# Kernel optimization log

Hardware: AMD Instinct MI355X
Metric: run time of the kernel (lower is better)

## Reference

```python
import jax, jax.numpy as jnp
import numpy as np

HEADS = 4
KS = 7          # neighborhood kernel size
EPS = 1e-5
C = 64
N, H, W = 8, 64, 64


def _gather_idx(L, k):
    # NATTEN-style neighborhood: window centered at pixel, shifted to stay in bounds.
    start = jnp.clip(jnp.arange(L) - k // 2, 0, L - k)            # [L]
    idx = start[:, None] + jnp.arange(k)                           # [L, k] absolute neighbor idx
    # relative-position-bias index: (query - neighbor) + (k-1) in [0, 2k-2]
    rel = (jnp.arange(L) - start)[:, None] + (k - 1) - jnp.arange(k)[None, :]  # [L, k]
    return idx, rel


def na2d(x, qkv_w, qkv_b, rpb, proj_w, proj_b):
    # x: [N, H, W, C] -> neighborhood attention with rel-pos bias
    n, h, w, c = x.shape
    hd = c // HEADS
    scale = hd ** -0.5
    qkv = (x @ qkv_w.T + qkv_b).reshape(n, h, w, 3, HEADS, hd)
    q = qkv[..., 0, :, :] * scale                                  # [n,h,w,heads,hd]
    k = qkv[..., 1, :, :]
    v = qkv[..., 2, :, :]
    idx_h, rel_h = _gather_idx(h, KS)
    idx_w, rel_w = _gather_idx(w, KS)
    # gather neighborhoods: [n, h, k, w, k, heads, hd]
    kg = k[:, idx_h][:, :, :, idx_w]
    vg = v[:, idx_h][:, :, :, idx_w]
    attn = jnp.einsum('nijhd,niajbhd->nijhab', q, kg)              # [n,h,w,heads,k,k]
    bias = rpb[:, rel_h, :]                                        # [heads, h, k, 2k-1]
    bias = jnp.take(bias, rel_w, axis=-1)                          # [heads, h, k, w, k]
    bias = jnp.transpose(bias, (1, 3, 0, 2, 4))                    # [h, w, heads, k, k]
    attn = attn + bias
    a = jax.nn.softmax(attn.reshape(n, h, w, HEADS, KS * KS), axis=-1).reshape(attn.shape)
    out = jnp.einsum('nijhab,niajbhd->nijhd', a, vg).reshape(n, h, w, c)
    return out @ proj_w.T + proj_b


def setup_inputs() -> dict:
    key = jax.random.key(0)
    ks = jax.random.split(key, 12)
    s = 0.02
    return {
        'x': jax.random.normal(ks[0], (N, C, H, W), jnp.float32),
        'gn_w': jnp.ones((C,), jnp.float32),
        'gn_b': jnp.zeros((C,), jnp.float32),
        'qkv_w': jax.random.normal(ks[1], (3 * C, C), jnp.float32) * s,
        'qkv_b': jnp.zeros((3 * C,), jnp.float32),
        'rpb': jax.random.normal(ks[2], (HEADS, 2 * KS - 1, 2 * KS - 1), jnp.float32) * s,
        'proj_w': jax.random.normal(ks[3], (C, C), jnp.float32) * s,
        'proj_b': jnp.zeros((C,), jnp.float32),
        'ln_w': jnp.ones((C,), jnp.float32),
        'ln_b': jnp.zeros((C,), jnp.float32),
        'fc1_w': jax.random.normal(ks[4], (4 * C, C), jnp.float32) * s,
        'fc1_b': jnp.zeros((4 * C,), jnp.float32),
        'fc2_w': jax.random.normal(ks[5], (C, 4 * C), jnp.float32) * s,
        'fc2_b': jnp.zeros((C,), jnp.float32),
    }


def reference(x, gn_w, gn_b, qkv_w, qkv_b, rpb, proj_w, proj_b,
              ln_w, ln_b, fc1_w, fc1_b, fc2_w, fc2_b):
    n, c, h, w = x.shape
    x1 = jnp.transpose(x, (0, 2, 3, 1))                            # residual, NHWC
    # GroupNorm(1, C): normalize over (C,H,W) per sample, per-channel affine
    mu = jnp.mean(x, axis=(1, 2, 3), keepdims=True)
    var = jnp.var(x, axis=(1, 2, 3), keepdims=True)
    xg = (x - mu) * jax.lax.rsqrt(var + EPS)
    xg = xg * gn_w[None, :, None, None] + gn_b[None, :, None, None]
    xg = jnp.transpose(xg, (0, 2, 3, 1))                           # NHWC
    y = na2d(xg, qkv_w, qkv_b, rpb, proj_w, proj_b) + x1           # [n,h,w,c]
    y = y.reshape(n, h * w, c)
    # LayerNorm over channels + MLP (GELU), residual
    mu2 = jnp.mean(y, axis=-1, keepdims=True)
    var2 = jnp.var(y, axis=-1, keepdims=True)
    yn = (y - mu2) * jax.lax.rsqrt(var2 + EPS) * ln_w + ln_b
    hdn = jax.nn.gelu(yn @ fc1_w.T + fc1_b, approximate=False)
    y = y + (hdn @ fc2_w.T + fc2_b)
    return jnp.transpose(y.reshape(n, h, w, c), (0, 3, 1, 2))      # back to NCHW
```

## Files before the change

kernel.cpp:

```cpp
#include <hip/hip_runtime.h>
#include <math.h>

#define NSAMP 8
#define CH 64
#define HH 64
#define WW 64
#define SPATIAL 4096
#define PER_SAMPLE 262144
#define NTOK 32768
#define NHEADS 4
#define HD 16
#define KS 7
#define EPS 1e-5f
#define QSCALE 0.25f

typedef __attribute__((ext_vector_type(8))) short short8;
typedef __attribute__((ext_vector_type(4))) float f32x4;

__device__ __forceinline__ unsigned short f2bf(float f) {
    unsigned u = __float_as_uint(f);
    u = u + 0x7fffu + ((u >> 16) & 1u);
    return (unsigned short)(u >> 16);
}
__device__ __forceinline__ unsigned pack2(float a, float b) {
    return (unsigned)f2bf(a) | ((unsigned)f2bf(b) << 16);
}
__device__ __forceinline__ float dot8_bf(uint4 u, const float* qv) {
    float s;
    s = __uint_as_float(u.x << 16) * qv[0];
    s = fmaf(__uint_as_float(u.x & 0xffff0000u), qv[1], s);
    s = fmaf(__uint_as_float(u.y << 16),         qv[2], s);
    s = fmaf(__uint_as_float(u.y & 0xffff0000u), qv[3], s);
    s = fmaf(__uint_as_float(u.z << 16),         qv[4], s);
    s = fmaf(__uint_as_float(u.z & 0xffff0000u), qv[5], s);
    s = fmaf(__uint_as_float(u.w << 16),         qv[6], s);
    s = fmaf(__uint_as_float(u.w & 0xffff0000u), qv[7], s);
    return s;
}
__device__ __forceinline__ void pv8_bf(uint4 u, float p, float* acc) {
    acc[0] = fmaf(p, __uint_as_float(u.x << 16),         acc[0]);
    acc[1] = fmaf(p, __uint_as_float(u.x & 0xffff0000u), acc[1]);
    acc[2] = fmaf(p, __uint_as_float(u.y << 16),         acc[2]);
    acc[3] = fmaf(p, __uint_as_float(u.y & 0xffff0000u), acc[3]);
    acc[4] = fmaf(p, __uint_as_float(u.z << 16),         acc[4]);
    acc[5] = fmaf(p, __uint_as_float(u.z & 0xffff0000u), acc[5]);
    acc[6] = fmaf(p, __uint_as_float(u.w << 16),         acc[6]);
    acc[7] = fmaf(p, __uint_as_float(u.w & 0xffff0000u), acc[7]);
}

__global__ __launch_bounds__(256) void k_statsprep(const float* __restrict__ x,
                                                   float* __restrict__ stats,
                                                   const float* __restrict__ qkv_w,
                                                   const float* __restrict__ fc1_w,
                                                   const float* __restrict__ fc2_w,
                                                   const float* __restrict__ proj_w,
                                                   unsigned short* __restrict__ wb) {
    int blk = blockIdx.x;
    if (blk >= 256) {
        int i = (blk - 256) * 256 + threadIdx.x;
        if (i < 12288)      wb[i] = f2bf(qkv_w[i]);
        else if (i < 28672) wb[i] = f2bf(fc1_w[i - 12288]);
        else if (i < 45056) wb[i] = f2bf(fc2_w[i - 28672]);
        else                wb[i] = f2bf(proj_w[i - 45056]);
        return;
    }
    int n = blk >> 5, chunk = blk & 31;
    const float4* p4 = (const float4*)(x + n * PER_SAMPLE + chunk * 8192);
    int t = threadIdx.x;
    float s1 = 0.f, s2 = 0.f;
#pragma unroll
    for (int i = 0; i < 8; i++) {
        float4 v = p4[t + i * 256];
        s1 += v.x + v.y + v.z + v.w;
        s2 += v.x * v.x + v.y * v.y + v.z * v.z + v.w * v.w;
    }
#pragma unroll
    for (int off = 1; off < 64; off <<= 1) {
        s1 += __shfl_xor(s1, off);
        s2 += __shfl_xor(s2, off);
    }
    __shared__ float r1[4], r2[4];
    int lane = t & 63, wv = t >> 6;
    if (lane == 0) { r1[wv] = s1; r2[wv] = s2; }
    __syncthreads();
    if (t == 0) {
        atomicAdd(&stats[n * 2 + 0], r1[0] + r1[1] + r1[2] + r1[3]);
        atomicAdd(&stats[n * 2 + 1], r2[0] + r2[1] + r2[2] + r2[3]);
    }
}

__global__ __launch_bounds__(256) void k_qkv(const float* __restrict__ x,
                                             const float* __restrict__ stats,
                                             const float* __restrict__ gn_w,
                                             const float* __restrict__ gn_b,
                                             const unsigned short* __restrict__ qkv_wb,
                                             const float* __restrict__ qkv_b,
                                             uint4* __restrict__ qb8,
                                             uint4* __restrict__ kvb8) {
    __shared__ __attribute__((aligned(16))) short xA[4 * 2 * 64 * 8];
    __shared__ float obuf[4][16 * 65];
    int s0 = blockIdx.x * 64;
    int smp = s0 >> 12, sp = s0 & 4095;
    int t = threadIdx.x, tok = t & 63, g = t >> 6;

    float mu = stats[2 * smp] * (1.f / (float)PER_SAMPLE);
    float var = stats[2 * smp + 1] * (1.f / (float)PER_SAMPLE) - mu * mu;
    float rstd = rsqrtf(var + EPS);

    {
        const float* xp = x + smp * PER_SAMPLE + sp + tok;
        float v[16];
#pragma unroll
        for (int i = 0; i < 16; i++) {
            int c = g * 16 + i;
            v[i] = (xp[(size_t)c * SPATIAL] - mu) * rstd * gn_w[c] + gn_b[c];
        }
#pragma unroll
        for (int e = 0; e < 2; e++) {
            int cb = 2 * g + e;
            int kf = cb >> 2, qq = cb & 3;
            uint4 p;
            p.x = pack2(v[e * 8 + 0], v[e * 8 + 1]);
            p.y = pack2(v[e * 8 + 2], v[e * 8 + 3]);
            p.z = pack2(v[e * 8 + 4], v[e * 8 + 5]);
            p.w = pack2(v[e * 8 + 6], v[e * 8 + 7]);
            int chunk = ((tok >> 4) * 2 + kf) * 64 + (tok & 15) + (qq << 4);
            *(uint4*)&xA[chunk * 8] = p;
        }
    }
    __syncthreads();

    int w = __builtin_amdgcn_readfirstlane(g);
    int lane = t & 63, nh = lane & 15, qd = lane >> 4;

    short8 af[8];
#pragma unroll
    for (int mt = 0; mt < 4; mt++)
#pragma unroll
        for (int kf = 0; kf < 2; kf++)
            af[mt * 2 + kf] = *(const short8*)&xA[((mt * 2 + kf) * 64 + lane) * 8];

    for (int nt = 0; nt < 3; nt++) {
        int n0 = w * 48 + nt * 16;
        const unsigned short* wp = qkv_wb + (size_t)(n0 + nh) * 64 + qd * 8;
        short8 b0 = *(const short8*)(wp);
        short8 b1 = *(const short8*)(wp + 32);
        float bias = qkv_b[n0 + nh];
        bool isq = (n0 < 64);
        f32x4 acc[4];
#pragma unroll
        for (int mt = 0; mt < 4; mt++) {
            f32x4 d = {0.f, 0.f, 0.f, 0.f};
            d = __builtin_amdgcn_mfma_f32_16x16x32_bf16(af[mt * 2 + 0], b0, d, 0, 0, 0);
            d = __builtin_amdgcn_mfma_f32_16x16x32_bf16(af[mt * 2 + 1], b1, d, 0, 0, 0);
            acc[mt] = d;
        }
#pragma unroll
        for (int mt = 0; mt < 4; mt++)
#pragma unroll
            for (int r = 0; r < 4; r++) {
                float vv = acc[mt][r] + bias;
                if (isq) vv *= QSCALE;
                obuf[w][nh * 65 + mt * 16 + qd * 4 + r] = vv;
            }
        __builtin_amdgcn_wave_barrier();
#pragma unroll
        for (int u = 0; u < 2; u++) {
            uint4 p;
            p.x = pack2(obuf[w][(u * 8 + 0) * 65 + lane], obuf[w][(u * 8 + 1) * 65 + lane]);
            p.y = pack2(obuf[w][(u * 8 + 2) * 65 + lane], obuf[w][(u * 8 + 3) * 65 + lane]);
            p.z = pack2(obuf[w][(u * 8 + 4) * 65 + lane], obuf[w][(u * 8 + 5) * 65 + lane]);
            p.w = pack2(obuf[w][(u * 8 + 6) * 65 + lane], obuf[w][(u * 8 + 7) * 65 + lane]);
            if (n0 < 64)
                qb8[(size_t)((n0 >> 3) + u) * NTOK + s0 + lane] = p;
            else if (n0 < 128)
                kvb8[(size_t)(((n0 - 64) >> 3) + u) * NTOK + s0 + lane] = p;
            else
                kvb8[(size_t)(8 + ((n0 - 128) >> 3) + u) * NTOK + s0 + lane] = p;
        }
        __builtin_amdgcn_wave_barrier();
    }
}

__global__ __launch_bounds__(256) void k_fused(const uint4* __restrict__ qb8,
                                               const uint4* __restrict__ kvb8,
                                               const float* __restrict__ rpb,
                                               const unsigned short* __restrict__ proj_wb,
                                               const float* __restrict__ proj_b,
                                               const float* __restrict__ x,
                                               const float* __restrict__ ln_w,
                                               const float* __restrict__ ln_b,
                                               const unsigned short* __restrict__ fc1_wb,
                                               const float* __restrict__ fc1_b,
                                               const unsigned short* __restrict__ fc2_wb,
                                               const float* __restrict__ fc2_b,
                                               float* __restrict__ out) {
    __shared__ __attribute__((aligned(16))) short fragA[4 * 2 * 64 * 8];
    __shared__ __attribute__((aligned(16))) short lhA[4 * 4 * 64 * 8];
    __shared__ float obuf[4][16 * 65];
    __shared__ float red1[256], red2[256];
    int xcd = blockIdx.x & 7, idx = blockIdx.x >> 3;
    int h = xcd * 8 + (idx & 7);
    int n = idx >> 3;
    int t = threadIdx.x, w = t & 63;
    int g = __builtin_amdgcn_readfirstlane(t >> 6);
    int rowbase = n * 4096 + h * 64;

    const float* xr = x + n * PER_SAMPLE + h * 64;
    float xres[16];
#pragma unroll
    for (int i = 0; i < 16; i++)
        xres[i] = xr[(size_t)(g * 16 + i) * SPATIAL + w];

    float q[16];
    {
        uint4 qa = qb8[(size_t)(2 * g) * NTOK + rowbase + w];
        uint4 qc = qb8[(size_t)(2 * g + 1) * NTOK + rowbase + w];
        q[0] = __uint_as_float(qa.x << 16); q[1] = __uint_as_float(qa.x & 0xffff0000u);
        q[2] = __uint_as_float(qa.y << 16); q[3] = __uint_as_float(qa.y & 0xffff0000u);
        q[4] = __uint_as_float(qa.z << 16); q[5] = __uint_as_float(qa.z & 0xffff0000u);
        q[6] = __uint_as_float(qa.w << 16); q[7] = __uint_as_float(qa.w & 0xffff0000u);
        q[8]  = __uint_as_float(qc.x << 16); q[9]  = __uint_as_float(qc.x & 0xffff0000u);
        q[10] = __uint_as_float(qc.y << 16); q[11] = __uint_as_float(qc.y & 0xffff0000u);
        q[12] = __uint_as_float(qc.z << 16); q[13] = __uint_as_float(qc.z & 0xffff0000u);
        q[14] = __uint_as_float(qc.w << 16); q[15] = __uint_as_float(qc.w & 0xffff0000u);
    }
    int sh = min(max(h - 3, 0), HH - KS);
    int sw = min(max(w - 3, 0), WW - KS);

    float lg[49];
    float mx = -1e30f;
#pragma unroll
    for (int a = 0; a < 7; a++) {
        int nb = n * 4096 + (sh + a) * 64 + sw;
        const float* rp = rpb + (g * 13 + (h - sh + 6 - a)) * 13;
#pragma unroll
        for (int bb = 0; bb < 7; bb++) {
            size_t base = (size_t)(2 * g) * NTOK + nb + bb;
            float d = dot8_bf(kvb8[base], q) + dot8_bf(kvb8[base + NTOK], q + 8);
            d += rp[w - sw + 6 - bb];
            lg[a * 7 + bb] = d;
            mx = fmaxf(mx, d);
        }
    }
    float sum = 0.f;
#pragma unroll
    for (int i = 0; i < 49; i++) {
        float e = __expf(lg[i] - mx);
        lg[i] = e;
        sum += e;
    }
    float rs = 1.f / sum;

    float acc[16];
#pragma unroll
    for (int i = 0; i < 16; i++) acc[i] = 0.f;
#pragma unroll
    for (int a = 0; a < 7; a++) {
        int nb = n * 4096 + (sh + a) * 64 + sw;
#pragma unroll
        for (int bb = 0; bb < 7; bb++) {
            size_t base = (size_t)(8 + 2 * g) * NTOK + nb + bb;
            float p = lg[a * 7 + bb];
            pv8_bf(kvb8[base], p, acc);
            pv8_bf(kvb8[base + NTOK], p, acc + 8);
        }
    }
#pragma unroll
    for (int e = 0; e < 2; e++) {
        int cb = 2 * g + e;
        int kf = cb >> 2, qq = cb & 3;
        uint4 p;
        p.x = pack2(acc[e * 8 + 0] * rs, acc[e * 8 + 1] * rs);
        p.y = pack2(acc[e * 8 + 2] * rs, acc[e * 8 + 3] * rs);
        p.z = pack2(acc[e * 8 + 4] * rs, acc[e * 8 + 5] * rs);
        p.w = pack2(acc[e * 8 + 6] * rs, acc[e * 8 + 7] * rs);
        int chunk = ((w >> 4) * 2 + kf) * 64 + (w & 15) + (qq << 4);
        *(uint4*)&fragA[chunk * 8] = p;
    }
    __syncthreads();

    int lane = t & 63, nh = lane & 15, qd = lane >> 4;
    float yreg[16];
    {
        short8 af[8];
#pragma unroll
        for (int mt = 0; mt < 4; mt++)
#pragma unroll
            for (int kf = 0; kf < 2; kf++)
                af[mt * 2 + kf] = *(const short8*)&fragA[((mt * 2 + kf) * 64 + lane) * 8];

        int n0 = g * 16;
        const unsigned short* wp = proj_wb + (size_t)(n0 + nh) * 64 + qd * 8;
        short8 b0 = *(const short8*)(wp);
        short8 b1 = *(const short8*)(wp + 32);
        float bias = proj_b[n0 + nh];
#pragma unroll
        for (int mt = 0; mt < 4; mt++) {
            f32x4 d = {0.f, 0.f, 0.f, 0.f};
            d = __builtin_amdgcn_mfma_f32_16x16x32_bf16(af[mt * 2 + 0], b0, d, 0, 0, 0);
            d = __builtin_amdgcn_mfma_f32_16x16x32_bf16(af[mt * 2 + 1], b1, d, 0, 0, 0);
#pragma unroll
            for (int r = 0; r < 4; r++)
                obuf[g][nh * 65 + mt * 16 + qd * 4 + r] = d[r] + bias;
        }
        __builtin_amdgcn_wave_barrier();
#pragma unroll
        for (int i = 0; i < 16; i++)
            yreg[i] = obuf[g][i * 65 + lane] + xres[i];
    }

    {
        float s1 = 0.f, s2 = 0.f;
#pragma unroll
        for (int i = 0; i < 16; i++) { s1 += yreg[i]; s2 += yreg[i] * yreg[i]; }
        red1[g * 64 + w] = s1;
        red2[g * 64 + w] = s2;
        __syncthreads();
        float mu = (red1[w] + red1[64 + w] + red1[128 + w] + red1[192 + w]) * (1.f / 64.f);
        float sq = (red2[w] + red2[64 + w] + red2[128 + w] + red2[192 + w]) * (1.f / 64.f);
        float rstd = rsqrtf(sq - mu * mu + EPS);
        float v[16];
#pragma unroll
        for (int i = 0; i < 16; i++) {
            int c = g * 16 + i;
            v[i] = (yreg[i] - mu) * rstd * ln_w[c] + ln_b[c];
        }
#pragma unroll
        for (int e = 0; e < 2; e++) {
            int cb = 2 * g + e;
            int kf = cb >> 2, qq = cb & 3;
            uint4 p;
            p.x = pack2(v[e * 8 + 0], v[e * 8 + 1]);
            p.y = pack2(v[e * 8 + 2], v[e * 8 + 3]);
            p.z = pack2(v[e * 8 + 4], v[e * 8 + 5]);
            p.w = pack2(v[e * 8 + 6], v[e * 8 + 7]);
            int chunk = ((w >> 4) * 2 + kf) * 64 + (w & 15) + (qq << 4);
            *(uint4*)&fragA[chunk * 8] = p;
        }
    }
    __syncthreads();

    short8 yf[8];
#pragma unroll
    for (int mt = 0; mt < 4; mt++)
#pragma unroll
        for (int kf = 0; kf < 2; kf++)
            yf[mt * 2 + kf] = *(const short8*)&fragA[((mt * 2 + kf) * 64 + lane) * 8];

    f32x4 acc2[4];
#pragma unroll
    for (int mt = 0; mt < 4; mt++) acc2[mt] = (f32x4){0.f, 0.f, 0.f, 0.f};

    for (int half = 0; half < 2; half++) {
#pragma unroll
        for (int nt = 0; nt < 2; nt++) {
            int n0f = half * 128 + g * 32 + nt * 16;
            const unsigned short* wp = fc1_wb + (size_t)(n0f + nh) * 64 + qd * 8;
            short8 b0 = *(const short8*)(wp);
            short8 b1 = *(const short8*)(wp + 32);
            float bias = fc1_b[n0f + nh];
            int j = n0f + nh;
            int kfl = (j - half * 128) >> 5;
            int q2 = (j >> 3) & 3, jb = j & 7;
#pragma unroll
            for (int mt = 0; mt < 4; mt++) {
                f32x4 d = {0.f, 0.f, 0.f, 0.f};
                d = __builtin_amdgcn_mfma_f32_16x16x32_bf16(yf[mt * 2 + 0], b0, d, 0, 0, 0);
                d = __builtin_amdgcn_mfma_f32_16x16x32_bf16(yf[mt * 2 + 1], b1, d, 0, 0, 0);
#pragma unroll
                for (int r = 0; r < 4; r++) {
                    float hv = d[r] + bias;
                    hv = 0.5f * hv * (1.f + erff(hv * 0.70710678118654752f));
                    lhA[(mt * 4 + kfl) * 512 + ((qd * 4 + r) + (q2 << 4)) * 8 + jb] = (short)f2bf(hv);
                }
            }
        }
        __syncthreads();
#pragma unroll
        for (int kf = 0; kf < 4; kf++) {
            int kfg = half * 4 + kf;
            const unsigned short* wp = fc2_wb + (size_t)(g * 16 + nh) * 256 + kfg * 32 + qd * 8;
            short8 bb = *(const short8*)(wp);
#pragma unroll
            for (int mt = 0; mt < 4; mt++) {
                short8 a = *(const short8*)&lhA[((mt * 4 + kf) * 64 + lane) * 8];
                acc2[mt] = __builtin_amdgcn_mfma_f32_16x16x32_bf16(a, bb, acc2[mt], 0, 0, 0);
            }
        }
        __syncthreads();
    }

#pragma unroll
    for (int mt = 0; mt < 4; mt++)
#pragma unroll
        for (int r = 0; r < 4; r++)
            obuf[g][nh * 65 + mt * 16 + qd * 4 + r] = acc2[mt][r];
    __builtin_amdgcn_wave_barrier();
    float* op = out + (size_t)n * PER_SAMPLE + h * 64;
#pragma unroll
    for (int u = 0; u < 4; u++) {
#pragma unroll
        for (int e = 0; e < 4; e++) {
            int c = g * 16 + u * 4 + e;
            op[(size_t)c * SPATIAL + lane] = obuf[g][(u * 4 + e) * 65 + lane]
                                           + fc2_b[c] + yreg[u * 4 + e];
        }
    }
}

extern "C" void kernel_launch(void* const* d_in, const int* in_sizes, int n_in,
                              void* d_out, int out_size, void* d_ws, size_t ws_size,
                              hipStream_t stream) {
    const float* x      = (const float*)d_in[0];
    const float* gn_w   = (const float*)d_in[1];
    const float* gn_b   = (const float*)d_in[2];
    const float* qkv_w  = (const float*)d_in[3];
    const float* qkv_b  = (const float*)d_in[4];
    const float* rpb    = (const float*)d_in[5];
    const float* proj_w = (const float*)d_in[6];
    const float* proj_b = (const float*)d_in[7];
    const float* ln_w   = (const float*)d_in[8];
    const float* ln_b   = (const float*)d_in[9];
    const float* fc1_w  = (const float*)d_in[10];
    const float* fc1_b  = (const float*)d_in[11];
    const float* fc2_w  = (const float*)d_in[12];
    const float* fc2_b  = (const float*)d_in[13];
    float* out = (float*)d_out;

    float* ws    = (float*)d_ws;
    float* stats = ws;
    uint4* qb8   = (uint4*)(ws + 64);
    uint4* kvb8  = qb8 + (size_t)8 * NTOK;
    unsigned short* wb = (unsigned short*)(kvb8 + (size_t)16 * NTOK);
    unsigned short* qkv_wb  = wb;
    unsigned short* fc1_wb  = wb + 12288;
    unsigned short* fc2_wb  = wb + 28672;
    unsigned short* proj_wb = wb + 45056;

    hipMemsetAsync(stats, 0, 64, stream);
    k_statsprep<<<448, 256, 0, stream>>>(x, stats, qkv_w, fc1_w, fc2_w, proj_w, wb);
    k_qkv      <<<512, 256, 0, stream>>>(x, stats, gn_w, gn_b, qkv_wb, qkv_b, qb8, kvb8);
    k_fused    <<<512, 256, 0, stream>>>(qb8, kvb8, rpb, proj_wb, proj_b, x,
                                         ln_w, ln_b, fc1_wb, fc1_b, fc2_wb, fc2_b, out);
}
```

Before: 139.9 us.

## Split fused attention+MLP kernel over half-rows with channel-split lanes

Each block now handles half an image row (32 pixels), and each wave splits its 16 head channels across two lane halves, combining the partial q·k dot products with a cross-lane shuffle. This halves per-thread register arrays (q, acc, xres, yreg, fragments) and doubles the grid to 1024 blocks, with a launch-bounds occupancy hint of 4 blocks per SM. The aim is more waves in flight to hide latency of the neighborhood gathers. In exchange, the MLP weight fragments are loaded by twice as many blocks and each neighbor needs an extra shuffle.

```diff
diff --git a/kernel.cpp b/kernel.cpp
--- a/kernel.cpp
+++ b/kernel.cpp
@@ -182,7 +182,7 @@
     }
 }
 
-__global__ __launch_bounds__(256) void k_fused(const uint4* __restrict__ qb8,
+__global__ __launch_bounds__(256, 4) void k_fused(const uint4* __restrict__ qb8,
                                                const uint4* __restrict__ kvb8,
                                                const float* __restrict__ rpb,
                                                const unsigned short* __restrict__ proj_wb,
@@ -195,35 +195,35 @@
                                                const unsigned short* __restrict__ fc2_wb,
                                                const float* __restrict__ fc2_b,
                                                float* __restrict__ out) {
-    __shared__ __attribute__((aligned(16))) short fragA[4 * 2 * 64 * 8];
-    __shared__ __attribute__((aligned(16))) short lhA[4 * 4 * 64 * 8];
-    __shared__ float obuf[4][16 * 65];
+    __shared__ __attribute__((aligned(16))) short fragA[2 * 2 * 64 * 8];
+    __shared__ __attribute__((aligned(16))) short lhA[2 * 8 * 64 * 8];
+    __shared__ float obuf[4][16 * 33];
     __shared__ float red1[256], red2[256];
     int xcd = blockIdx.x & 7, idx = blockIdx.x >> 3;
-    int h = xcd * 8 + (idx & 7);
-    int n = idx >> 3;
-    int t = threadIdx.x, w = t & 63;
+    int half = idx & 1;
+    int h = xcd * 8 + ((idx >> 1) & 7);
+    int n = idx >> 4;
+    int t = threadIdx.x, lane = t & 63;
     int g = __builtin_amdgcn_readfirstlane(t >> 6);
+    int w2 = lane & 31;
+    int dh = lane >> 5;
+    int w = half * 32 + w2;
     int rowbase = n * 4096 + h * 64;
-
-    const float* xr = x + n * PER_SAMPLE + h * 64;
-    float xres[16];
-#pragma unroll
-    for (int i = 0; i < 16; i++)
-        xres[i] = xr[(size_t)(g * 16 + i) * SPATIAL + w];
-
-    float q[16];
-    {
-        uint4 qa = qb8[(size_t)(2 * g) * NTOK + rowbase + w];
-        uint4 qc = qb8[(size_t)(2 * g + 1) * NTOK + rowbase + w];
+    int cb = 2 * g + dh;
+
+    const float* xr = x + n * PER_SAMPLE + h * 64 + w;
+    float xres[8];
+#pragma unroll
+    for (int i = 0; i < 8; i++)
+        xres[i] = xr[(size_t)(cb * 8 + i) * SPATIAL];
+
+    float q[8];
+    {
+        uint4 qa = qb8[(size_t)cb * NTOK + rowbase + w];
         q[0] = __uint_as_float(qa.x << 16); q[1] = __uint_as_float(qa.x & 0xffff0000u);
         q[2] = __uint_as_float(qa.y << 16); q[3] = __uint_as_float(qa.y & 0xffff0000u);
         q[4] = __uint_as_float(qa.z << 16); q[5] = __uint_as_float(qa.z & 0xffff0000u);
         q[6] = __uint_as_float(qa.w << 16); q[7] = __uint_as_float(qa.w & 0xffff0000u);
-        q[8]  = __uint_as_float(qc.x << 16); q[9]  = __uint_as_float(qc.x & 0xffff0000u);
-        q[10] = __uint_as_float(qc.y << 16); q[11] = __uint_as_float(qc.y & 0xffff0000u);
-        q[12] = __uint_as_float(qc.z << 16); q[13] = __uint_as_float(qc.z & 0xffff0000u);
-        q[14] = __uint_as_float(qc.w << 16); q[15] = __uint_as_float(qc.w & 0xffff0000u);
     }
     int sh = min(max(h - 3, 0), HH - KS);
     int sw = min(max(w - 3, 0), WW - KS);
@@ -236,8 +236,8 @@
         const float* rp = rpb + (g * 13 + (h - sh + 6 - a)) * 13;
 #pragma unroll
         for (int bb = 0; bb < 7; bb++) {
-            size_t base = (size_t)(2 * g) * NTOK + nb + bb;
-            float d = dot8_bf(kvb8[base], q) + dot8_bf(kvb8[base + NTOK], q + 8);
+            float dhalf = dot8_bf(kvb8[(size_t)cb * NTOK + nb + bb], q);
+            float d = dhalf + __shfl_xor(dhalf, 32);
             d += rp[w - sw + 6 - bb];
             lg[a * 7 + bb] = d;
             mx = fmaxf(mx, d);
@@ -252,40 +252,33 @@
     }
     float rs = 1.f / sum;
 
-    float acc[16];
-#pragma unroll
-    for (int i = 0; i < 16; i++) acc[i] = 0.f;
+    float acc[8];
+#pragma unroll
+    for (int i = 0; i < 8; i++) acc[i] = 0.f;
 #pragma unroll
     for (int a = 0; a < 7; a++) {
         int nb = n * 4096 + (sh + a) * 64 + sw;
 #pragma unroll
-        for (int bb = 0; bb < 7; bb++) {
-            size_t base = (size_t)(8 + 2 * g) * NTOK + nb + bb;
-            float p = lg[a * 7 + bb];
-            pv8_bf(kvb8[base], p, acc);
-            pv8_bf(kvb8[base + NTOK], p, acc + 8);
-        }
-    }
-#pragma unroll
-    for (int e = 0; e < 2; e++) {
-        int cb = 2 * g + e;
-        int kf = cb >> 2, qq = cb & 3;
+        for (int bb = 0; bb < 7; bb++)
+            pv8_bf(kvb8[(size_t)(8 + cb) * NTOK + nb + bb], lg[a * 7 + bb], acc);
+    }
+    {
+        int kf = cb >> 2, qsel = cb & 3;
         uint4 p;
-        p.x = pack2(acc[e * 8 + 0] * rs, acc[e * 8 + 1] * rs);
-        p.y = pack2(acc[e * 8 + 2] * rs, acc[e * 8 + 3] * rs);
-        p.z = pack2(acc[e * 8 + 4] * rs, acc[e * 8 + 5] * rs);
-        p.w = pack2(acc[e * 8 + 6] * rs, acc[e * 8 + 7] * rs);
-        int chunk = ((w >> 4) * 2 + kf) * 64 + (w & 15) + (qq << 4);
-        *(uint4*)&fragA[chunk * 8] = p;
+        p.x = pack2(acc[0] * rs, acc[1] * rs);
+        p.y = pack2(acc[2] * rs, acc[3] * rs);
+        p.z = pack2(acc[4] * rs, acc[5] * rs);
+        p.w = pack2(acc[6] * rs, acc[7] * rs);
+        *(uint4*)&fragA[(((w2 >> 4) * 2 + kf) * 64 + (w2 & 15) + (qsel << 4)) * 8] = p;
     }
     __syncthreads();
 
-    int lane = t & 63, nh = lane & 15, qd = lane >> 4;
-    float yreg[16];
-    {
-        short8 af[8];
-#pragma unroll
-        for (int mt = 0; mt < 4; mt++)
+    int nh = lane & 15, qd = lane >> 4;
+    float yreg[8];
+    {
+        short8 af[4];
+#pragma unroll
+        for (int mt = 0; mt < 2; mt++)
 #pragma unroll
             for (int kf = 0; kf < 2; kf++)
                 af[mt * 2 + kf] = *(const short8*)&fragA[((mt * 2 + kf) * 64 + lane) * 8];
@@ -296,75 +289,67 @@
         short8 b1 = *(const short8*)(wp + 32);
         float bias = proj_b[n0 + nh];
 #pragma unroll
-        for (int mt = 0; mt < 4; mt++) {
+        for (int mt = 0; mt < 2; mt++) {
             f32x4 d = {0.f, 0.f, 0.f, 0.f};
             d = __builtin_amdgcn_mfma_f32_16x16x32_bf16(af[mt * 2 + 0], b0, d, 0, 0, 0);
             d = __builtin_amdgcn_mfma_f32_16x16x32_bf16(af[mt * 2 + 1], b1, d, 0, 0, 0);
 #pragma unroll
             for (int r = 0; r < 4; r++)
-                obuf[g][nh * 65 + mt * 16 + qd * 4 + r] = d[r] + bias;
+                obuf[g][nh * 33 + mt * 16 + qd * 4 + r] = d[r] + bias;
         }
         __builtin_amdgcn_wave_barrier();
 #pragma unroll
-        for (int i = 0; i < 16; i++)
-            yreg[i] = obuf[g][i * 65 + lane] + xres[i];
+        for (int i = 0; i < 8; i++)
+            yreg[i] = obuf[g][(dh * 8 + i) * 33 + w2] + xres[i];
     }
 
     {
         float s1 = 0.f, s2 = 0.f;
 #pragma unroll
-        for (int i = 0; i < 16; i++) { s1 += yreg[i]; s2 += yreg[i] * yreg[i]; }
-        red1[g * 64 + w] = s1;
-        red2[g * 64 + w] = s2;
+        for (int i = 0; i < 8; i++) { s1 += yreg[i]; s2 += yreg[i] * yreg[i]; }
+        red1[t] = s1;
+        red2[t] = s2;
         __syncthreads();
-        float mu = (red1[w] + red1[64 + w] + red1[128 + w] + red1[192 + w]) * (1.f / 64.f);
-        float sq = (red2[w] + red2[64 + w] + red2[128 + w] + red2[192 + w]) * (1.f / 64.f);
-        float rstd = rsqrtf(sq - mu * mu + EPS);
-        float v[16];
-#pragma unroll
-        for (int i = 0; i < 16; i++) {
-            int c = g * 16 + i;
+        float m1 = 0.f, m2 = 0.f;
+#pragma unroll
+        for (int u = 0; u < 8; u++) { m1 += red1[u * 32 + w2]; m2 += red2[u * 32 + w2]; }
+        float mu = m1 * (1.f / 64.f);
+        float rstd = rsqrtf(m2 * (1.f / 64.f) - mu * mu + EPS);
+        float v[8];
+#pragma unroll
+        for (int i = 0; i < 8; i++) {
+            int c = cb * 8 + i;
             v[i] = (yreg[i] - mu) * rstd * ln_w[c] + ln_b[c];
         }
-#pragma unroll
-        for (int e = 0; e < 2; e++) {
-            int cb = 2 * g + e;
-            int kf = cb >> 2, qq = cb & 3;
-            uint4 p;
-            p.x = pack2(v[e * 8 + 0], v[e * 8 + 1]);
-            p.y = pack2(v[e * 8 + 2], v[e * 8 + 3]);
-            p.z = pack2(v[e * 8 + 4], v[e * 8 + 5]);
-            p.w = pack2(v[e * 8 + 6], v[e * 8 + 7]);
-            int chunk = ((w >> 4) * 2 + kf) * 64 + (w & 15) + (qq << 4);
-            *(uint4*)&fragA[chunk * 8] = p;
-        }
+        int kf = cb >> 2, qsel = cb & 3;
+        uint4 p;
+        p.x = pack2(v[0], v[1]);
+        p.y = pack2(v[2], v[3]);
+        p.z = pack2(v[4], v[5]);
+        p.w = pack2(v[6], v[7]);
+        *(uint4*)&fragA[(((w2 >> 4) * 2 + kf) * 64 + (w2 & 15) + (qsel << 4)) * 8] = p;
     }
     __syncthreads();
 
-    short8 yf[8];
-#pragma unroll
-    for (int mt = 0; mt < 4; mt++)
-#pragma unroll
-        for (int kf = 0; kf < 2; kf++)
-            yf[mt * 2 + kf] = *(const short8*)&fragA[((mt * 2 + kf) * 64 + lane) * 8];
-
-    f32x4 acc2[4];
-#pragma unroll
-    for (int mt = 0; mt < 4; mt++) acc2[mt] = (f32x4){0.f, 0.f, 0.f, 0.f};
-
-    for (int half = 0; half < 2; half++) {
-#pragma unroll
-        for (int nt = 0; nt < 2; nt++) {
-            int n0f = half * 128 + g * 32 + nt * 16;
+    {
+        short8 yf[4];
+#pragma unroll
+        for (int mt = 0; mt < 2; mt++)
+#pragma unroll
+            for (int kf = 0; kf < 2; kf++)
+                yf[mt * 2 + kf] = *(const short8*)&fragA[((mt * 2 + kf) * 64 + lane) * 8];
+
+#pragma unroll
+        for (int nt = 0; nt < 4; nt++) {
+            int n0f = g * 64 + nt * 16;
             const unsigned short* wp = fc1_wb + (size_t)(n0f + nh) * 64 + qd * 8;
             short8 b0 = *(const short8*)(wp);
             short8 b1 = *(const short8*)(wp + 32);
             float bias = fc1_b[n0f + nh];
             int j = n0f + nh;
-            int kfl = (j - half * 128) >> 5;
-            int q2 = (j >> 3) & 3, jb = j & 7;
-#pragma unroll
-            for (int mt = 0; mt < 4; mt++) {
+            int kfA = j >> 5, q2 = (j >> 3) & 3, jb = j & 7;
+#pragma unroll
+            for (int mt = 0; mt < 2; mt++) {
                 f32x4 d = {0.f, 0.f, 0.f, 0.f};
                 d = __builtin_amdgcn_mfma_f32_16x16x32_bf16(yf[mt * 2 + 0], b0, d, 0, 0, 0);
                 d = __builtin_amdgcn_mfma_f32_16x16x32_bf16(yf[mt * 2 + 1], b1, d, 0, 0, 0);
@@ -372,40 +357,37 @@
                 for (int r = 0; r < 4; r++) {
                     float hv = d[r] + bias;
                     hv = 0.5f * hv * (1.f + erff(hv * 0.70710678118654752f));
-                    lhA[(mt * 4 + kfl) * 512 + ((qd * 4 + r) + (q2 << 4)) * 8 + jb] = (short)f2bf(hv);
+                    lhA[((mt * 8 + kfA) * 64 + (qd * 4 + r) + (q2 << 4)) * 8 + jb] = (short)f2bf(hv);
                 }
             }
         }
-        __syncthreads();
-#pragma unroll
-        for (int kf = 0; kf < 4; kf++) {
-            int kfg = half * 4 + kf;
-            const unsigned short* wp = fc2_wb + (size_t)(g * 16 + nh) * 256 + kfg * 32 + qd * 8;
-            short8 bb = *(const short8*)(wp);
-#pragma unroll
-            for (int mt = 0; mt < 4; mt++) {
-                short8 a = *(const short8*)&lhA[((mt * 4 + kf) * 64 + lane) * 8];
-                acc2[mt] = __builtin_amdgcn_mfma_f32_16x16x32_bf16(a, bb, acc2[mt], 0, 0, 0);
-            }
-        }
-        __syncthreads();
-    }
-
-#pragma unroll
-    for (int mt = 0; mt < 4; mt++)
+    }
+    __syncthreads();
+
+    f32x4 acc2[2];
+    acc2[0] = (f32x4){0.f, 0.f, 0.f, 0.f};
+    acc2[1] = (f32x4){0.f, 0.f, 0.f, 0.f};
+#pragma unroll
+    for (int kfA = 0; kfA < 8; kfA++) {
+        const unsigned short* wp = fc2_wb + (size_t)(g * 16 + nh) * 256 + kfA * 32 + qd * 8;
+        short8 bb = *(const short8*)(wp);
+#pragma unroll
+        for (int mt = 0; mt < 2; mt++) {
+            short8 a = *(const short8*)&lhA[((mt * 8 + kfA) * 64 + lane) * 8];
+            acc2[mt] = __builtin_amdgcn_mfma_f32_16x16x32_bf16(a, bb, acc2[mt], 0, 0, 0);
+        }
+    }
+#pragma unroll
+    for (int mt = 0; mt < 2; mt++)
 #pragma unroll
         for (int r = 0; r < 4; r++)
-            obuf[g][nh * 65 + mt * 16 + qd * 4 + r] = acc2[mt][r];
+            obuf[g][nh * 33 + mt * 16 + qd * 4 + r] = acc2[mt][r];
     __builtin_amdgcn_wave_barrier();
-    float* op = out + (size_t)n * PER_SAMPLE + h * 64;
-#pragma unroll
-    for (int u = 0; u < 4; u++) {
-#pragma unroll
-        for (int e = 0; e < 4; e++) {
-            int c = g * 16 + u * 4 + e;
-            op[(size_t)c * SPATIAL + lane] = obuf[g][(u * 4 + e) * 65 + lane]
-                                           + fc2_b[c] + yreg[u * 4 + e];
-        }
+    float* op = out + (size_t)n * PER_SAMPLE + h * 64 + w;
+#pragma unroll
+    for (int i = 0; i < 8; i++) {
+        int c = cb * 8 + i;
+        op[(size_t)c * SPATIAL] = obuf[g][(dh * 8 + i) * 33 + w2] + fc2_b[c] + yreg[i];
     }
 }
 
@@ -441,6 +423,6 @@
     hipMemsetAsync(stats, 0, 64, stream);
     k_statsprep<<<448, 256, 0, stream>>>(x, stats, qkv_w, fc1_w, fc2_w, proj_w, wb);
     k_qkv      <<<512, 256, 0, stream>>>(x, stats, gn_w, gn_b, qkv_wb, qkv_b, qb8, kvb8);
-    k_fused    <<<512, 256, 0, stream>>>(qb8, kvb8, rpb, proj_wb, proj_b, x,
-                                         ln_w, ln_b, fc1_wb, fc1_b, fc2_wb, fc2_b, out);
-}
+    k_fused    <<<1024, 256, 0, stream>>>(qb8, kvb8, rpb, proj_wb, proj_b, x,
+                                          ln_w, ln_b, fc1_wb, fc1_b, fc2_wb, fc2_b, out);
+}
```

Measured after the change: 133.2 us. 4.8% less time.
